# Performance work log

Hardware: AMD Instinct MI355X
Metric: run time of the kernel (lower is better)

The kernel has to match this reference:

```python
import jax, jax.numpy as jnp
import numpy as np


def setup_inputs() -> dict:
    key = jax.random.key(0)
    k1, k2, k3, k4 = jax.random.split(key, 4)
    B, N, F, T, K, O = 16, 1024, 16, 12, 3, 16
    x = jax.random.normal(k1, (B, N, F, T), dtype=jnp.float32)
    spatial_attention = jax.random.uniform(k2, (B, N, N), dtype=jnp.float32)
    adj = jax.random.uniform(k3, (N, N), dtype=jnp.float32)
    # xavier_uniform_ on [K, F, O]: bound = sqrt(6/(F+O)) over last two dims
    bound = float(np.sqrt(6.0 / (F + O)))
    Theta = jax.random.uniform(k4, (K, F, O), dtype=jnp.float32, minval=-bound, maxval=bound)
    return {"x": x, "spatial_attention": spatial_attention, "adj": adj, "Theta": Theta}


def reference(x, spatial_attention, adj, Theta):
    # x: [B, N, F, T], spatial_attention: [B, N, N], adj: [N, N], Theta: [K, F, O]
    B, N, F, T = x.shape
    K = Theta.shape[0]
    a = adj[None, :, :] * spatial_attention                      # [B, N, N]
    eye = jnp.broadcast_to(jnp.eye(N, dtype=x.dtype), (B, N, N))
    supports = [eye, a]
    for _ in range(2, K):                                        # power series of adjacency
        supports.append(jnp.matmul(supports[-1], a))
    S = jnp.stack(supports, axis=0)                              # [K, B, N, N]
    # rhs[k,b,n,f,t] = sum_m S[k,b,m,n] * x[b,m,f,t]  (supports[k]^T @ x), fused over T and K
    rhs = jnp.einsum('kbmn,bmft->kbnft', S, x)                   # [K, B, N, F, T]
    out = jnp.einsum('kbnft,kfo->bnot', rhs, Theta)              # [B, N, O, T]
    return jax.nn.relu(out)
```

## Files before the change

kernel.cpp:

```cpp
#include <hip/hip_runtime.h>
#include <hip/hip_bf16.h>


typedef __attribute__((ext_vector_type(8))) __bf16 bf16x8;
typedef __attribute__((ext_vector_type(4))) float  f32x4;
typedef __attribute__((ext_vector_type(8))) short  short8;

__device__ inline unsigned short f32_to_bf16(float f) {
    unsigned int u = __builtin_bit_cast(unsigned int, f);
    unsigned int r = u + 0x7FFFu + ((u >> 16) & 1u);
    return (unsigned short)(r >> 16);
}
__device__ inline float bf16_to_f32(unsigned short u) {
    unsigned int x = ((unsigned int)u) << 16;
    return __builtin_bit_cast(float, x);
}

__device__ inline void gload_lds16(const void* gsrc, void* ldst) {
    __builtin_amdgcn_global_load_lds(
        (const __attribute__((address_space(1))) unsigned int*)gsrc,
        (__attribute__((address_space(3))) unsigned int*)ldst,
        16, 0, 0);
}

__global__ void prep_a(const float* __restrict__ sa, const float* __restrict__ adj,
                       unsigned short* __restrict__ aT)
{
    __shared__ float tile[32][33];
    const int b  = blockIdx.z;
    const int m0 = blockIdx.y * 32;
    const int n0 = blockIdx.x * 32;
    const int tid = threadIdx.x;
    const int c  = tid & 31;
    const int r4 = tid >> 5;
    const float* sab = sa + (size_t)b * 1024 * 1024;
#pragma unroll
    for (int i = 0; i < 4; i++) {
        int rr = r4 + i * 8;
        size_t idx = (size_t)(m0 + rr) * 1024 + (n0 + c);
        tile[rr][c] = adj[idx] * sab[idx];
    }
    __syncthreads();
    unsigned short* aTb = aT + (size_t)b * 1024 * 1024;
#pragma unroll
    for (int i = 0; i < 4; i++) {
        int rr = r4 + i * 8;
        aTb[(size_t)(n0 + rr) * 1024 + (m0 + c)] = f32_to_bf16(tile[c][rr]);
    }
}

__global__ void prep_x(const float* __restrict__ x, unsigned short* __restrict__ xT)
{
    __shared__ float tile[32][33];
    const int b  = blockIdx.z;
    const int j0 = blockIdx.y * 32;
    const int m0 = blockIdx.x * 32;
    const int tid = threadIdx.x;
    const int c  = tid & 31;
    const int r4 = tid >> 5;
    const float* xb = x + (size_t)b * 1024 * 192;
#pragma unroll
    for (int i = 0; i < 4; i++) {
        int rr = r4 + i * 8;
        tile[rr][c] = xb[(size_t)(m0 + rr) * 192 + (j0 + c)];
    }
    __syncthreads();
    unsigned short* xTb = xT + (size_t)b * 192 * 1024;
#pragma unroll
    for (int i = 0; i < 4; i++) {
        int rr = r4 + i * 8;
        xTb[(size_t)(j0 + rr) * 1024 + (m0 + c)] = f32_to_bf16(tile[c][rr]);
    }
}

__global__ __launch_bounds__(256, 1)
void gemm_tn(const unsigned short* __restrict__ Aop,
             const unsigned short* __restrict__ Bop,
             unsigned short* __restrict__ Cout)
{
    const int b  = blockIdx.z;
    const int j0 = blockIdx.y * 96;
    const int n0 = blockIdx.x * 128;
    const unsigned short* Ab = Aop + (size_t)b * 192 * 1024;
    const unsigned short* Bb = Bop + (size_t)b * 1024 * 1024;

    __shared__ unsigned short Blds[3][128 * 64];

    const int tid  = threadIdx.x;
    const int lane = tid & 63;
    const int wave = tid >> 6;
    const int wj   = wave >> 1;
    const int wn   = wave & 1;
    const int lr   = lane & 15;
    const int lg   = lane >> 4;

    const int srow = lane >> 3;
    const int sg16 = (lane & 7) ^ srow;

    f32x4 acc[3][4];
#pragma unroll
    for (int i = 0; i < 3; i++)
#pragma unroll
        for (int j = 0; j < 4; j++) acc[i][j] = f32x4{0.f, 0.f, 0.f, 0.f};

    const unsigned short* Arow[3];
#pragma unroll
    for (int ri = 0; ri < 3; ri++)
        Arow[ri] = Ab + (size_t)(j0 + wj * 48 + ri * 16 + lr) * 1024 + lg * 8;

    bf16x8 Ac[2][3], An[2][3];

#pragma unroll
    for (int i = 0; i < 4; i++) {
        int c = wave * 4 + i;
        gload_lds16(Bb + (size_t)(n0 + 8 * c + srow) * 1024 + 0 + sg16 * 8,
                    &Blds[0][c * 512]);
    }
#pragma unroll
    for (int i = 0; i < 4; i++) {
        int c = wave * 4 + i;
        gload_lds16(Bb + (size_t)(n0 + 8 * c + srow) * 1024 + 64 + sg16 * 8,
                    &Blds[1][c * 512]);
    }
#pragma unroll
    for (int h = 0; h < 2; h++)
#pragma unroll
        for (int ri = 0; ri < 3; ri++)
            Ac[h][ri] = __builtin_bit_cast(bf16x8,
                *reinterpret_cast<const short8*>(Arow[ri] + h * 32));
    __builtin_amdgcn_sched_barrier(0);
    asm volatile("s_waitcnt vmcnt(10)" ::: "memory");
    __builtin_amdgcn_s_barrier();
    __builtin_amdgcn_sched_barrier(0);

#pragma unroll
    for (int t = 0; t < 16; ++t) {
        const unsigned short* ldsB = &Blds[t % 3][0];
        bf16x8 Bfr[2][4];
#pragma unroll
        for (int h = 0; h < 2; h++)
#pragma unroll
            for (int ci = 0; ci < 4; ci++) {
                int row = wn * 64 + ci * 16 + lr;
                int sw  = (h * 4 + lg) ^ (lr & 7);
                Bfr[h][ci] = __builtin_bit_cast(bf16x8,
                    *reinterpret_cast<const short8*>(ldsB + row * 64 + sw * 8));
            }
        if (t < 14) {
#pragma unroll
            for (int i = 0; i < 4; i++) {
                int c = wave * 4 + i;
                gload_lds16(Bb + (size_t)(n0 + 8 * c + srow) * 1024 + (t + 2) * 64 + sg16 * 8,
                            &Blds[(t + 2) % 3][c * 512]);
            }
        }
        if (t < 15) {
#pragma unroll
            for (int h = 0; h < 2; h++)
#pragma unroll
                for (int ri = 0; ri < 3; ri++)
                    An[h][ri] = __builtin_bit_cast(bf16x8,
                        *reinterpret_cast<const short8*>(Arow[ri] + (t + 1) * 64 + h * 32));
        }
#pragma unroll
        for (int h = 0; h < 2; h++)
#pragma unroll
            for (int ri = 0; ri < 3; ri++)
#pragma unroll
                for (int ci = 0; ci < 4; ci++)
                    acc[ri][ci] = __builtin_amdgcn_mfma_f32_16x16x32_bf16(
                        Ac[h][ri], Bfr[h][ci], acc[ri][ci], 0, 0, 0);
#pragma unroll
        for (int h = 0; h < 2; h++)
#pragma unroll
            for (int ri = 0; ri < 3; ri++)
                Ac[h][ri] = An[h][ri];
        asm volatile("s_waitcnt vmcnt(10)" ::: "memory");
        __builtin_amdgcn_s_barrier();
        __builtin_amdgcn_sched_barrier(0);
    }

    unsigned short* Cb = Cout + (size_t)b * 192 * 1024;
    const int jw = j0 + wj * 48;
    const int nw = n0 + wn * 64;
#pragma unroll
    for (int ri = 0; ri < 3; ri++)
#pragma unroll
        for (int ci = 0; ci < 4; ci++) {
            int col = nw + ci * 16 + lr;
#pragma unroll
            for (int r = 0; r < 4; r++) {
                int row = jw + ri * 16 + lg * 4 + r;
                Cb[(size_t)row * 1024 + col] = f32_to_bf16(acc[ri][ci][r]);
            }
        }
}

#define OBUF_STRIDE 196

__global__ __launch_bounds__(192)
void final_contract(const unsigned short* __restrict__ xT,
                    const unsigned short* __restrict__ r1,
                    const unsigned short* __restrict__ r2,
                    const float* __restrict__ Theta,
                    float* __restrict__ out)
{
    __shared__ float th[768];
    __shared__ float obuf[64 * OBUF_STRIDE];

    const int tid = threadIdx.x;
    for (int i = tid; i < 768; i += 192) th[i] = Theta[i];
    __syncthreads();

    const int b  = blockIdx.y;
    const int n0 = blockIdx.x * 64;
    const int nl = tid & 63;
    const int tq = tid >> 6;

    float acc[4][16];
#pragma unroll
    for (int tt = 0; tt < 4; tt++)
#pragma unroll
        for (int o = 0; o < 16; o++) acc[tt][o] = 0.f;

    const size_t basep = (size_t)b * 192 * 1024 + n0 + nl;
#pragma unroll
    for (int f = 0; f < 16; f++) {
        size_t off = basep + (size_t)(f * 12 + tq * 4) * 1024;
        float v0[4], v1[4], v2[4];
#pragma unroll
        for (int tt = 0; tt < 4; tt++) {
            v0[tt] = bf16_to_f32(xT[off + (size_t)tt * 1024]);
            v1[tt] = bf16_to_f32(r1[off + (size_t)tt * 1024]);
            v2[tt] = bf16_to_f32(r2[off + (size_t)tt * 1024]);
        }
        const f32x4* t0 = reinterpret_cast<const f32x4*>(&th[0 * 256 + f * 16]);
        const f32x4* t1 = reinterpret_cast<const f32x4*>(&th[1 * 256 + f * 16]);
        const f32x4* t2 = reinterpret_cast<const f32x4*>(&th[2 * 256 + f * 16]);
#pragma unroll
        for (int q = 0; q < 4; q++) {
            f32x4 w0 = t0[q], w1 = t1[q], w2 = t2[q];
#pragma unroll
            for (int tt = 0; tt < 4; tt++)
#pragma unroll
                for (int e = 0; e < 4; e++)
                    acc[tt][q * 4 + e] += v0[tt] * w0[e] + v1[tt] * w1[e] + v2[tt] * w2[e];
        }
    }
#pragma unroll
    for (int o = 0; o < 16; o++) {
        f32x4 v;
#pragma unroll
        for (int tt = 0; tt < 4; tt++) v[tt] = fmaxf(acc[tt][o], 0.f);
        *reinterpret_cast<f32x4*>(&obuf[nl * OBUF_STRIDE + o * 12 + tq * 4]) = v;
    }
    __syncthreads();

    float* outp = out + ((size_t)b * 1024 + n0) * 192;
#pragma unroll
    for (int i = 0; i < 16; i++) {
        int v   = tid + i * 192;
        int row = v / 48;
        int c   = v - row * 48;
        *reinterpret_cast<f32x4*>(&outp[(size_t)v * 4]) =
            *reinterpret_cast<const f32x4*>(&obuf[row * OBUF_STRIDE + c * 4]);
    }
}

extern "C" void kernel_launch(void* const* d_in, const int* in_sizes, int n_in,
                              void* d_out, int out_size, void* d_ws, size_t ws_size,
                              hipStream_t stream)
{
    const float* x     = (const float*)d_in[0];
    const float* sa    = (const float*)d_in[1];
    const float* adj   = (const float*)d_in[2];
    const float* Theta = (const float*)d_in[3];
    float* out = (float*)d_out;

    char* ws = (char*)d_ws;
    const size_t SZ_AT = (size_t)16 * 1024 * 1024 * 2;
    const size_t SZ_XT = (size_t)16 * 192  * 1024 * 2;
    unsigned short* aT = (unsigned short*)ws;
    unsigned short* xT = (unsigned short*)(ws + SZ_AT);
    unsigned short* r1 = (unsigned short*)(ws + SZ_AT + SZ_XT);
    unsigned short* r2 = (unsigned short*)(ws + SZ_AT + 2 * SZ_XT);

    prep_a<<<dim3(32, 32, 16), 256, 0, stream>>>(sa, adj, aT);
    prep_x<<<dim3(32, 6, 16), 256, 0, stream>>>(x, xT);
    gemm_tn<<<dim3(8, 2, 16), 256, 0, stream>>>(xT, aT, r1);
    gemm_tn<<<dim3(8, 2, 16), 256, 0, stream>>>(r1, aT, r2);
    final_contract<<<dim3(16, 16), 192, 0, stream>>>(xT, r1, r2, Theta, out);
}
```

Before: 76.62 us.

## Halve GEMM N-tile to double block count and vectorize prep transposes

The GEMM N tile shrinks from 128 to 64 columns, doubling the grid from 256 to 512 blocks and allowing two blocks per CU. This should fill more of the 256 CUs and hide latency, but each block now reuses its A fragments over fewer columns, so A traffic per output rises. The prep transpose kernels switch to 16-byte float4 loads and 8-byte packed bf16 stores to cut memory instruction count.

```diff
diff --git a/kernel.cpp b/kernel.cpp
--- a/kernel.cpp
+++ b/kernel.cpp
@@ -5,6 +5,7 @@
 typedef __attribute__((ext_vector_type(8))) __bf16 bf16x8;
 typedef __attribute__((ext_vector_type(4))) float  f32x4;
 typedef __attribute__((ext_vector_type(8))) short  short8;
+typedef __attribute__((ext_vector_type(4))) short  s16x4;
 
 __device__ inline unsigned short f32_to_bf16(float f) {
     unsigned int u = __builtin_bit_cast(unsigned int, f);
@@ -31,22 +32,24 @@
     const int m0 = blockIdx.y * 32;
     const int n0 = blockIdx.x * 32;
     const int tid = threadIdx.x;
-    const int c  = tid & 31;
-    const int r4 = tid >> 5;
+    const int r  = tid >> 3;
+    const int c4 = (tid & 7) * 4;
     const float* sab = sa + (size_t)b * 1024 * 1024;
-#pragma unroll
-    for (int i = 0; i < 4; i++) {
-        int rr = r4 + i * 8;
-        size_t idx = (size_t)(m0 + rr) * 1024 + (n0 + c);
-        tile[rr][c] = adj[idx] * sab[idx];
-    }
-    __syncthreads();
+
+    size_t idx = (size_t)(m0 + r) * 1024 + (n0 + c4);
+    f32x4 av = *reinterpret_cast<const f32x4*>(&adj[idx]);
+    f32x4 sv = *reinterpret_cast<const f32x4*>(&sab[idx]);
+#pragma unroll
+    for (int k = 0; k < 4; k++) tile[r][c4 + k] = av[k] * sv[k];
+    __syncthreads();
+
     unsigned short* aTb = aT + (size_t)b * 1024 * 1024;
-#pragma unroll
-    for (int i = 0; i < 4; i++) {
-        int rr = r4 + i * 8;
-        aTb[(size_t)(n0 + rr) * 1024 + (m0 + c)] = f32_to_bf16(tile[c][rr]);
-    }
+    const int nl = tid >> 3;
+    const int m4 = (tid & 7) * 4;
+    s16x4 v;
+#pragma unroll
+    for (int k = 0; k < 4; k++) v[k] = (short)f32_to_bf16(tile[m4 + k][nl]);
+    *reinterpret_cast<s16x4*>(&aTb[(size_t)(n0 + nl) * 1024 + m0 + m4]) = v;
 }
 
 __global__ void prep_x(const float* __restrict__ x, unsigned short* __restrict__ xT)
@@ -56,35 +59,36 @@
     const int j0 = blockIdx.y * 32;
     const int m0 = blockIdx.x * 32;
     const int tid = threadIdx.x;
-    const int c  = tid & 31;
-    const int r4 = tid >> 5;
+    const int r  = tid >> 3;
+    const int c4 = (tid & 7) * 4;
     const float* xb = x + (size_t)b * 1024 * 192;
-#pragma unroll
-    for (int i = 0; i < 4; i++) {
-        int rr = r4 + i * 8;
-        tile[rr][c] = xb[(size_t)(m0 + rr) * 192 + (j0 + c)];
-    }
-    __syncthreads();
+
+    f32x4 v = *reinterpret_cast<const f32x4*>(&xb[(size_t)(m0 + r) * 192 + j0 + c4]);
+#pragma unroll
+    for (int k = 0; k < 4; k++) tile[r][c4 + k] = v[k];
+    __syncthreads();
+
     unsigned short* xTb = xT + (size_t)b * 192 * 1024;
-#pragma unroll
-    for (int i = 0; i < 4; i++) {
-        int rr = r4 + i * 8;
-        xTb[(size_t)(j0 + rr) * 1024 + (m0 + c)] = f32_to_bf16(tile[c][rr]);
-    }
-}
-
-__global__ __launch_bounds__(256, 1)
+    const int jl = tid >> 3;
+    const int m4 = (tid & 7) * 4;
+    s16x4 o;
+#pragma unroll
+    for (int k = 0; k < 4; k++) o[k] = (short)f32_to_bf16(tile[m4 + k][jl]);
+    *reinterpret_cast<s16x4*>(&xTb[(size_t)(j0 + jl) * 1024 + m0 + m4]) = o;
+}
+
+__global__ __launch_bounds__(256, 2)
 void gemm_tn(const unsigned short* __restrict__ Aop,
              const unsigned short* __restrict__ Bop,
              unsigned short* __restrict__ Cout)
 {
     const int b  = blockIdx.z;
     const int j0 = blockIdx.y * 96;
-    const int n0 = blockIdx.x * 128;
+    const int n0 = blockIdx.x * 64;
     const unsigned short* Ab = Aop + (size_t)b * 192 * 1024;
     const unsigned short* Bb = Bop + (size_t)b * 1024 * 1024;
 
-    __shared__ unsigned short Blds[3][128 * 64];
+    __shared__ unsigned short Blds[3][64 * 64];
 
     const int tid  = threadIdx.x;
     const int lane = tid & 63;
@@ -97,11 +101,11 @@
     const int srow = lane >> 3;
     const int sg16 = (lane & 7) ^ srow;
 
-    f32x4 acc[3][4];
+    f32x4 acc[3][2];
 #pragma unroll
     for (int i = 0; i < 3; i++)
 #pragma unroll
-        for (int j = 0; j < 4; j++) acc[i][j] = f32x4{0.f, 0.f, 0.f, 0.f};
+        for (int j = 0; j < 2; j++) acc[i][j] = f32x4{0.f, 0.f, 0.f, 0.f};
 
     const unsigned short* Arow[3];
 #pragma unroll
@@ -111,14 +115,14 @@
     bf16x8 Ac[2][3], An[2][3];
 
 #pragma unroll
-    for (int i = 0; i < 4; i++) {
-        int c = wave * 4 + i;
+    for (int i = 0; i < 2; i++) {
+        int c = wave + i * 4;
         gload_lds16(Bb + (size_t)(n0 + 8 * c + srow) * 1024 + 0 + sg16 * 8,
                     &Blds[0][c * 512]);
     }
 #pragma unroll
-    for (int i = 0; i < 4; i++) {
-        int c = wave * 4 + i;
+    for (int i = 0; i < 2; i++) {
+        int c = wave + i * 4;
         gload_lds16(Bb + (size_t)(n0 + 8 * c + srow) * 1024 + 64 + sg16 * 8,
                     &Blds[1][c * 512]);
     }
@@ -129,27 +133,27 @@
             Ac[h][ri] = __builtin_bit_cast(bf16x8,
                 *reinterpret_cast<const short8*>(Arow[ri] + h * 32));
     __builtin_amdgcn_sched_barrier(0);
-    asm volatile("s_waitcnt vmcnt(10)" ::: "memory");
+    asm volatile("s_waitcnt vmcnt(8)" ::: "memory");
     __builtin_amdgcn_s_barrier();
     __builtin_amdgcn_sched_barrier(0);
 
 #pragma unroll
     for (int t = 0; t < 16; ++t) {
         const unsigned short* ldsB = &Blds[t % 3][0];
-        bf16x8 Bfr[2][4];
+        bf16x8 Bfr[2][2];
 #pragma unroll
         for (int h = 0; h < 2; h++)
 #pragma unroll
-            for (int ci = 0; ci < 4; ci++) {
-                int row = wn * 64 + ci * 16 + lr;
+            for (int ci = 0; ci < 2; ci++) {
+                int row = wn * 32 + ci * 16 + lr;
                 int sw  = (h * 4 + lg) ^ (lr & 7);
                 Bfr[h][ci] = __builtin_bit_cast(bf16x8,
                     *reinterpret_cast<const short8*>(ldsB + row * 64 + sw * 8));
             }
         if (t < 14) {
 #pragma unroll
-            for (int i = 0; i < 4; i++) {
-                int c = wave * 4 + i;
+            for (int i = 0; i < 2; i++) {
+                int c = wave + i * 4;
                 gload_lds16(Bb + (size_t)(n0 + 8 * c + srow) * 1024 + (t + 2) * 64 + sg16 * 8,
                             &Blds[(t + 2) % 3][c * 512]);
             }
@@ -167,7 +171,7 @@
 #pragma unroll
             for (int ri = 0; ri < 3; ri++)
 #pragma unroll
-                for (int ci = 0; ci < 4; ci++)
+                for (int ci = 0; ci < 2; ci++)
                     acc[ri][ci] = __builtin_amdgcn_mfma_f32_16x16x32_bf16(
                         Ac[h][ri], Bfr[h][ci], acc[ri][ci], 0, 0, 0);
 #pragma unroll
@@ -175,18 +179,18 @@
 #pragma unroll
             for (int ri = 0; ri < 3; ri++)
                 Ac[h][ri] = An[h][ri];
-        asm volatile("s_waitcnt vmcnt(10)" ::: "memory");
+        asm volatile("s_waitcnt vmcnt(8)" ::: "memory");
         __builtin_amdgcn_s_barrier();
         __builtin_amdgcn_sched_barrier(0);
     }
 
     unsigned short* Cb = Cout + (size_t)b * 192 * 1024;
     const int jw = j0 + wj * 48;
-    const int nw = n0 + wn * 64;
+    const int nw = n0 + wn * 32;
 #pragma unroll
     for (int ri = 0; ri < 3; ri++)
 #pragma unroll
-        for (int ci = 0; ci < 4; ci++) {
+        for (int ci = 0; ci < 2; ci++) {
             int col = nw + ci * 16 + lr;
 #pragma unroll
             for (int r = 0; r < 4; r++) {
@@ -287,7 +291,7 @@
 
     prep_a<<<dim3(32, 32, 16), 256, 0, stream>>>(sa, adj, aT);
     prep_x<<<dim3(32, 6, 16), 256, 0, stream>>>(x, xT);
-    gemm_tn<<<dim3(8, 2, 16), 256, 0, stream>>>(xT, aT, r1);
-    gemm_tn<<<dim3(8, 2, 16), 256, 0, stream>>>(r1, aT, r2);
+    gemm_tn<<<dim3(16, 2, 16), 256, 0, stream>>>(xT, aT, r1);
+    gemm_tn<<<dim3(16, 2, 16), 256, 0, stream>>>(r1, aT, r2);
     final_contract<<<dim3(16, 16), 192, 0, stream>>>(xT, r1, r2, Theta, out);
 }
```

Result: slower. 95.14 us (+24.2%).

## Retile gemm_tn to 192x64 tiles with 8 waves and swizzled block order

Applied to the files above, without the earlier changes.

The GEMM tile changes from 96x128 with 4 waves to the full 192 rows by 64 columns with 8 waves. Each wave now covers a 48x32 sub-tile, and each A operand row is loaded once per block instead of being split across two blocks. Block indices are swizzled so that consecutive blocks map to different batches and column tiles. The intent is to cut redundant A reads and improve L2/HBM locality, at the cost of fewer MFMAs per B-fragment load, which lowers compute intensity per wave.

```diff
diff --git a/kernel.cpp b/kernel.cpp
--- a/kernel.cpp
+++ b/kernel.cpp
@@ -73,18 +73,21 @@
     }
 }
 
-__global__ __launch_bounds__(256, 1)
+__global__ __launch_bounds__(512, 1)
 void gemm_tn(const unsigned short* __restrict__ Aop,
              const unsigned short* __restrict__ Bop,
              unsigned short* __restrict__ Cout)
 {
-    const int b  = blockIdx.z;
-    const int j0 = blockIdx.y * 96;
-    const int n0 = blockIdx.x * 128;
+    const int lin = blockIdx.x + 16 * blockIdx.y;
+    const int swz = (lin & 7) * 32 + (lin >> 3);
+    const int nb  = swz & 15;
+    const int b   = swz >> 4;
+
+    const int n0 = nb * 64;
     const unsigned short* Ab = Aop + (size_t)b * 192 * 1024;
     const unsigned short* Bb = Bop + (size_t)b * 1024 * 1024;
 
-    __shared__ unsigned short Blds[3][128 * 64];
+    __shared__ unsigned short Blds[3][64 * 64];
 
     const int tid  = threadIdx.x;
     const int lane = tid & 63;
@@ -97,31 +100,23 @@
     const int srow = lane >> 3;
     const int sg16 = (lane & 7) ^ srow;
 
-    f32x4 acc[3][4];
+    f32x4 acc[3][2];
 #pragma unroll
     for (int i = 0; i < 3; i++)
 #pragma unroll
-        for (int j = 0; j < 4; j++) acc[i][j] = f32x4{0.f, 0.f, 0.f, 0.f};
+        for (int j = 0; j < 2; j++) acc[i][j] = f32x4{0.f, 0.f, 0.f, 0.f};
 
     const unsigned short* Arow[3];
 #pragma unroll
     for (int ri = 0; ri < 3; ri++)
-        Arow[ri] = Ab + (size_t)(j0 + wj * 48 + ri * 16 + lr) * 1024 + lg * 8;
+        Arow[ri] = Ab + (size_t)(wj * 48 + ri * 16 + lr) * 1024 + lg * 8;
 
     bf16x8 Ac[2][3], An[2][3];
 
-#pragma unroll
-    for (int i = 0; i < 4; i++) {
-        int c = wave * 4 + i;
-        gload_lds16(Bb + (size_t)(n0 + 8 * c + srow) * 1024 + 0 + sg16 * 8,
-                    &Blds[0][c * 512]);
-    }
-#pragma unroll
-    for (int i = 0; i < 4; i++) {
-        int c = wave * 4 + i;
-        gload_lds16(Bb + (size_t)(n0 + 8 * c + srow) * 1024 + 64 + sg16 * 8,
-                    &Blds[1][c * 512]);
-    }
+    gload_lds16(Bb + (size_t)(n0 + 8 * wave + srow) * 1024 + 0 + sg16 * 8,
+                &Blds[0][wave * 512]);
+    gload_lds16(Bb + (size_t)(n0 + 8 * wave + srow) * 1024 + 64 + sg16 * 8,
+                &Blds[1][wave * 512]);
 #pragma unroll
     for (int h = 0; h < 2; h++)
 #pragma unroll
@@ -129,30 +124,26 @@
             Ac[h][ri] = __builtin_bit_cast(bf16x8,
                 *reinterpret_cast<const short8*>(Arow[ri] + h * 32));
     __builtin_amdgcn_sched_barrier(0);
-    asm volatile("s_waitcnt vmcnt(10)" ::: "memory");
+    asm volatile("s_waitcnt vmcnt(7)" ::: "memory");
     __builtin_amdgcn_s_barrier();
     __builtin_amdgcn_sched_barrier(0);
 
 #pragma unroll
     for (int t = 0; t < 16; ++t) {
         const unsigned short* ldsB = &Blds[t % 3][0];
-        bf16x8 Bfr[2][4];
+        bf16x8 Bfr[2][2];
 #pragma unroll
         for (int h = 0; h < 2; h++)
 #pragma unroll
-            for (int ci = 0; ci < 4; ci++) {
-                int row = wn * 64 + ci * 16 + lr;
+            for (int ci = 0; ci < 2; ci++) {
+                int row = wn * 32 + ci * 16 + lr;
                 int sw  = (h * 4 + lg) ^ (lr & 7);
                 Bfr[h][ci] = __builtin_bit_cast(bf16x8,
                     *reinterpret_cast<const short8*>(ldsB + row * 64 + sw * 8));
             }
         if (t < 14) {
-#pragma unroll
-            for (int i = 0; i < 4; i++) {
-                int c = wave * 4 + i;
-                gload_lds16(Bb + (size_t)(n0 + 8 * c + srow) * 1024 + (t + 2) * 64 + sg16 * 8,
-                            &Blds[(t + 2) % 3][c * 512]);
-            }
+            gload_lds16(Bb + (size_t)(n0 + 8 * wave + srow) * 1024 + (t + 2) * 64 + sg16 * 8,
+                        &Blds[(t + 2) % 3][wave * 512]);
         }
         if (t < 15) {
 #pragma unroll
@@ -167,7 +158,7 @@
 #pragma unroll
             for (int ri = 0; ri < 3; ri++)
 #pragma unroll
-                for (int ci = 0; ci < 4; ci++)
+                for (int ci = 0; ci < 2; ci++)
                     acc[ri][ci] = __builtin_amdgcn_mfma_f32_16x16x32_bf16(
                         Ac[h][ri], Bfr[h][ci], acc[ri][ci], 0, 0, 0);
 #pragma unroll
@@ -175,18 +166,18 @@
 #pragma unroll
             for (int ri = 0; ri < 3; ri++)
                 Ac[h][ri] = An[h][ri];
-        asm volatile("s_waitcnt vmcnt(10)" ::: "memory");
+        asm volatile("s_waitcnt vmcnt(7)" ::: "memory");
         __builtin_amdgcn_s_barrier();
         __builtin_amdgcn_sched_barrier(0);
     }
 
     unsigned short* Cb = Cout + (size_t)b * 192 * 1024;
-    const int jw = j0 + wj * 48;
-    const int nw = n0 + wn * 64;
+    const int jw = wj * 48;
+    const int nw = n0 + wn * 32;
 #pragma unroll
     for (int ri = 0; ri < 3; ri++)
 #pragma unroll
-        for (int ci = 0; ci < 4; ci++) {
+        for (int ci = 0; ci < 2; ci++) {
             int col = nw + ci * 16 + lr;
 #pragma unroll
             for (int r = 0; r < 4; r++) {
@@ -287,7 +278,7 @@
 
     prep_a<<<dim3(32, 32, 16), 256, 0, stream>>>(sa, adj, aT);
     prep_x<<<dim3(32, 6, 16), 256, 0, stream>>>(x, xT);
-    gemm_tn<<<dim3(8, 2, 16), 256, 0, stream>>>(xT, aT, r1);
-    gemm_tn<<<dim3(8, 2, 16), 256, 0, stream>>>(r1, aT, r2);
+    gemm_tn<<<dim3(16, 16), 512, 0, stream>>>(xT, aT, r1);
+    gemm_tn<<<dim3(16, 16), 512, 0, stream>>>(r1, aT, r2);
     final_contract<<<dim3(16, 16), 192, 0, stream>>>(xT, r1, r2, Theta, out);
 }
```

After: 94.22 us. 1.23x slower.

## Deepen GEMM prefetch pipeline to five LDS stages and remap blocks per XCD

Applied to the files above, without the earlier changes.

The batched bf16 GEMM now keeps five B-tile LDS buffers instead of three, staging tiles four steps ahead. A fragments are register-prefetched two steps ahead instead of one, which hides more global-load latency behind the MFMA work. It also remaps the linear block id so that consecutive hardware-scheduled blocks, which land on the same XCD, cover the same batch and share L2 reuse of the adjacency operand. The per-iteration explicit vmcnt wait was removed, so correctness of LDS reads now depends on compiler-inserted waits for the LDS-DMA loads. The change also raises LDS use and register pressure.

```diff
diff --git a/kernel.cpp b/kernel.cpp
--- a/kernel.cpp
+++ b/kernel.cpp
@@ -78,13 +78,18 @@
              const unsigned short* __restrict__ Bop,
              unsigned short* __restrict__ Cout)
 {
-    const int b  = blockIdx.z;
-    const int j0 = blockIdx.y * 96;
-    const int n0 = blockIdx.x * 128;
+    const int lin = blockIdx.x + 8 * (blockIdx.y + 2 * blockIdx.z);
+    const int swz = (lin & 7) * 32 + (lin >> 3);
+    const int nb  = swz & 7;
+    const int jb  = (swz >> 3) & 1;
+    const int b   = swz >> 4;
+
+    const int j0 = jb * 96;
+    const int n0 = nb * 128;
     const unsigned short* Ab = Aop + (size_t)b * 192 * 1024;
     const unsigned short* Bb = Bop + (size_t)b * 1024 * 1024;
 
-    __shared__ unsigned short Blds[3][128 * 64];
+    __shared__ unsigned short Blds[5][128 * 64];
 
     const int tid  = threadIdx.x;
     const int lane = tid & 63;
@@ -108,34 +113,37 @@
     for (int ri = 0; ri < 3; ri++)
         Arow[ri] = Ab + (size_t)(j0 + wj * 48 + ri * 16 + lr) * 1024 + lg * 8;
 
-    bf16x8 Ac[2][3], An[2][3];
-
-#pragma unroll
-    for (int i = 0; i < 4; i++) {
-        int c = wave * 4 + i;
-        gload_lds16(Bb + (size_t)(n0 + 8 * c + srow) * 1024 + 0 + sg16 * 8,
-                    &Blds[0][c * 512]);
-    }
-#pragma unroll
-    for (int i = 0; i < 4; i++) {
-        int c = wave * 4 + i;
-        gload_lds16(Bb + (size_t)(n0 + 8 * c + srow) * 1024 + 64 + sg16 * 8,
-                    &Blds[1][c * 512]);
-    }
-#pragma unroll
-    for (int h = 0; h < 2; h++)
-#pragma unroll
-        for (int ri = 0; ri < 3; ri++)
-            Ac[h][ri] = __builtin_bit_cast(bf16x8,
-                *reinterpret_cast<const short8*>(Arow[ri] + h * 32));
+    bf16x8 Ac[2][3], An[2][3], Ann[2][3];
+
+#define STAGE_TILE(T) \
+    { _Pragma("unroll") \
+      for (int i_ = 0; i_ < 4; i_++) { \
+          int c_ = wave * 4 + i_; \
+          gload_lds16(Bb + (size_t)(n0 + 8 * c_ + srow) * 1024 + (T) * 64 + sg16 * 8, \
+                      &Blds[(T) % 5][c_ * 512]); \
+      } }
+#define LOAD_A(DST, T) \
+    { _Pragma("unroll") \
+      for (int h_ = 0; h_ < 2; h_++) \
+          _Pragma("unroll") \
+          for (int ri_ = 0; ri_ < 3; ri_++) \
+              DST[h_][ri_] = __builtin_bit_cast(bf16x8, \
+                  *reinterpret_cast<const short8*>(Arow[ri_] + (T) * 64 + h_ * 32)); }
+
+    STAGE_TILE(0)
+    STAGE_TILE(1)
+    STAGE_TILE(2)
+    LOAD_A(Ac, 0)
+    STAGE_TILE(3)
+    LOAD_A(An, 1)
     __builtin_amdgcn_sched_barrier(0);
-    asm volatile("s_waitcnt vmcnt(10)" ::: "memory");
+    asm volatile("s_waitcnt vmcnt(24)" ::: "memory");
     __builtin_amdgcn_s_barrier();
     __builtin_amdgcn_sched_barrier(0);
 
 #pragma unroll
     for (int t = 0; t < 16; ++t) {
-        const unsigned short* ldsB = &Blds[t % 3][0];
+        const unsigned short* ldsB = &Blds[t % 5][0];
         bf16x8 Bfr[2][4];
 #pragma unroll
         for (int h = 0; h < 2; h++)
@@ -146,22 +154,9 @@
                 Bfr[h][ci] = __builtin_bit_cast(bf16x8,
                     *reinterpret_cast<const short8*>(ldsB + row * 64 + sw * 8));
             }
-        if (t < 14) {
-#pragma unroll
-            for (int i = 0; i < 4; i++) {
-                int c = wave * 4 + i;
-                gload_lds16(Bb + (size_t)(n0 + 8 * c + srow) * 1024 + (t + 2) * 64 + sg16 * 8,
-                            &Blds[(t + 2) % 3][c * 512]);
-            }
-        }
-        if (t < 15) {
-#pragma unroll
-            for (int h = 0; h < 2; h++)
-#pragma unroll
-                for (int ri = 0; ri < 3; ri++)
-                    An[h][ri] = __builtin_bit_cast(bf16x8,
-                        *reinterpret_cast<const short8*>(Arow[ri] + (t + 1) * 64 + h * 32));
-        }
+        if (t < 14) LOAD_A(Ann, t + 2)
+        __builtin_amdgcn_sched_barrier(0);
+        if (t < 12) STAGE_TILE(t + 4)
 #pragma unroll
         for (int h = 0; h < 2; h++)
 #pragma unroll
@@ -173,9 +168,10 @@
 #pragma unroll
         for (int h = 0; h < 2; h++)
 #pragma unroll
-            for (int ri = 0; ri < 3; ri++)
+            for (int ri = 0; ri < 3; ri++) {
                 Ac[h][ri] = An[h][ri];
-        asm volatile("s_waitcnt vmcnt(10)" ::: "memory");
+                An[h][ri] = Ann[h][ri];
+            }
         __builtin_amdgcn_s_barrier();
         __builtin_amdgcn_sched_barrier(0);
     }
@@ -194,6 +190,8 @@
                 Cb[(size_t)row * 1024 + col] = f32_to_bf16(acc[ri][ci][r]);
             }
         }
+#undef STAGE_TILE
+#undef LOAD_A
 }
 
 #define OBUF_STRIDE 196
```

After: 79.60 us. 1.04x slower.
